# Performance work log

Measured on AMD Instinct MI355X. Metric: run time of the kernel, lower is better.

The kernel has to match this reference:

```python
import jax, jax.numpy as jnp
import numpy as np

B = 131072   # batch of cells
D = 128      # input_dim == number of per-node models
OUTDIM = 2   # predict_var=True -> (delta, var) heads per node


def setup_inputs() -> dict:
    key = jax.random.key(0)
    k1, k2, k3 = jax.random.split(key, 3)
    state = jax.random.normal(k1, (B, D), dtype=jnp.float32)
    # Stacked weights of the D tiny Linear(D, 2) layers: W[n] is node n's [2, D] weight
    W = jax.random.normal(k2, (D, OUTDIM, D), dtype=jnp.float32) * 0.05
    b = jax.random.normal(k3, (D, OUTDIM), dtype=jnp.float32) * 0.05
    return {"state": state, "W": W, "b": b}


def reference(state, W, b):
    # Original: for each node i, y = Linear_i(state) -> delta[:, i] = y[:, 0]; var[:, i] = y[:, 1]
    # Batched equivalent: one einsum over all nodes at once.
    out = jnp.einsum('bd,nod->bno', state, W) + b  # [B, D, 2]
    delta = out[:, :, 0]
    var = out[:, :, 1]
    return delta, var
```

## Files before the change

kernel.cpp:

```cpp
#include <hip/hip_runtime.h>
#include <hip/hip_bf16.h>

typedef __attribute__((ext_vector_type(8))) short bf16x8;
typedef __attribute__((ext_vector_type(4))) float f32x4;

constexpr int BROWS = 131072;
constexpr int DDIM  = 128;

__device__ __forceinline__ short to_bf16(float f) {
    unsigned u = __builtin_bit_cast(unsigned, f);
    u = (u + 0x7FFFu + ((u >> 16) & 1u)) >> 16;
    return (short)u;
}

__device__ __forceinline__ bf16x8 cvt8(const float* __restrict__ p) {
    f32x4 lo = *reinterpret_cast<const f32x4*>(p);
    f32x4 hi = *reinterpret_cast<const f32x4*>(p + 4);
    bf16x8 r;
#pragma unroll
    for (int i = 0; i < 4; ++i) { r[i] = to_bf16(lo[i]); r[i + 4] = to_bf16(hi[i]); }
    return r;
}

__global__ void __launch_bounds__(256)
lfm_kernel(const float* __restrict__ state, const float* __restrict__ W,
           const float* __restrict__ bias, float* __restrict__ out) {
    const int lane = threadIdx.x & 63;
    const int wave = threadIdx.x >> 6;
    const int l16  = lane & 15;
    const int lq   = lane >> 4;

    const int colbase = wave * 64;
    bf16x8 wfrag[4][4];
    float  biasr[4];
#pragma unroll
    for (int ct = 0; ct < 4; ++ct) {
        const int c = colbase + ct * 16 + l16;
        const int n = c & 127, o = c >> 7;
        const float* wrow = W + n * 256 + o * 128;
        biasr[ct] = bias[n * 2 + o];
#pragma unroll
        for (int ks = 0; ks < 4; ++ks)
            wfrag[ct][ks] = cvt8(wrow + ks * 32 + lq * 8);
    }

    const int ntiles = BROWS / 16;
    for (int t = blockIdx.x; t < ntiles; t += gridDim.x) {
        const float* srow = state + (size_t)(t * 16 + l16) * DDIM;
        bf16x8 afrag[4];
#pragma unroll
        for (int ks = 0; ks < 4; ++ks)
            afrag[ks] = cvt8(srow + ks * 32 + lq * 8);

#pragma unroll
        for (int ct = 0; ct < 4; ++ct) {
            f32x4 acc = { biasr[ct], biasr[ct], biasr[ct], biasr[ct] };
#pragma unroll
            for (int ks = 0; ks < 4; ++ks)
                acc = __builtin_amdgcn_mfma_f32_16x16x32_bf16(
                        afrag[ks], wfrag[ct][ks], acc, 0, 0, 0);

            const int c = colbase + ct * 16 + l16;
            const size_t row = (size_t)t * 16 + lq * 4;
            float* dst = out + ((c < 128)
                                ? (row * 128 + c)
                                : ((size_t)BROWS * 128 + row * 128 + (c - 128)));
#pragma unroll
            for (int r = 0; r < 4; ++r)
                dst[(size_t)r * 128] = acc[r];
        }
    }
}

extern "C" void kernel_launch(void* const* d_in, const int* in_sizes, int n_in,
                              void* d_out, int out_size, void* d_ws, size_t ws_size,
                              hipStream_t stream) {
    const float* state = (const float*)d_in[0];
    const float* W     = (const float*)d_in[1];
    const float* bias  = (const float*)d_in[2];
    float* out = (float*)d_out;
    hipLaunchKernelGGL(lfm_kernel, dim3(2048), dim3(256), 0, stream,
                       state, W, bias, out);
}
```

Measured before the change: 221.9 us.

## Split output planes across blocks, swap MFMA operands for vector stores, double-buffer loads

Each block now handles only one output plane (delta or var), so each wave holds half the weight fragments. Swapping the MFMA operand order makes each lane own four contiguous output columns, which allows 16-byte vector stores in place of strided scalar stores. The tile loop is fully unrolled with two raw fp32 register buffers, so the next tile's state loads are in flight during the current tile's compute. The cost is that every state row is now read by two blocks, relying on L2 to absorb the duplicate traffic, and the code hardcodes an exact iteration count per block.

```diff
diff --git a/kernel.cpp b/kernel.cpp
--- a/kernel.cpp
+++ b/kernel.cpp
@@ -1,11 +1,13 @@
 #include <hip/hip_runtime.h>
-#include <hip/hip_bf16.h>
 
 typedef __attribute__((ext_vector_type(8))) short bf16x8;
 typedef __attribute__((ext_vector_type(4))) float f32x4;
 
 constexpr int BROWS = 131072;
 constexpr int DDIM  = 128;
+constexpr int NTILES = BROWS / 16;
+constexpr int CLSBLOCKS = 2048;
+constexpr int ITERS = NTILES / CLSBLOCKS;
 
 __device__ __forceinline__ short to_bf16(float f) {
     unsigned u = __builtin_bit_cast(unsigned, f);
@@ -13,16 +15,14 @@
     return (short)u;
 }
 
-__device__ __forceinline__ bf16x8 cvt8(const float* __restrict__ p) {
-    f32x4 lo = *reinterpret_cast<const f32x4*>(p);
-    f32x4 hi = *reinterpret_cast<const f32x4*>(p + 4);
+__device__ __forceinline__ bf16x8 cvt8(f32x4 lo, f32x4 hi) {
     bf16x8 r;
 #pragma unroll
     for (int i = 0; i < 4; ++i) { r[i] = to_bf16(lo[i]); r[i + 4] = to_bf16(hi[i]); }
     return r;
 }
 
-__global__ void __launch_bounds__(256)
+__global__ void __launch_bounds__(256, 4)
 lfm_kernel(const float* __restrict__ state, const float* __restrict__ W,
            const float* __restrict__ bias, float* __restrict__ out) {
     const int lane = threadIdx.x & 63;
@@ -30,46 +30,61 @@
     const int l16  = lane & 15;
     const int lq   = lane >> 4;
 
-    const int colbase = wave * 64;
-    bf16x8 wfrag[4][4];
-    float  biasr[4];
+    const int cls = blockIdx.x & 1;
+    const int tb  = blockIdx.x >> 1;
+    const int colbase = wave * 32;
+
+    bf16x8 wfrag[2][4];
+    f32x4  bias4[2];
 #pragma unroll
-    for (int ct = 0; ct < 4; ++ct) {
-        const int c = colbase + ct * 16 + l16;
-        const int n = c & 127, o = c >> 7;
-        const float* wrow = W + n * 256 + o * 128;
-        biasr[ct] = bias[n * 2 + o];
+    for (int ct = 0; ct < 2; ++ct) {
+        const int n = colbase + ct * 16 + l16;
+        const float* wrow = W + n * 256 + cls * 128;
 #pragma unroll
-        for (int ks = 0; ks < 4; ++ks)
-            wfrag[ct][ks] = cvt8(wrow + ks * 32 + lq * 8);
+        for (int ks = 0; ks < 4; ++ks) {
+            f32x4 lo = *reinterpret_cast<const f32x4*>(wrow + ks * 32 + lq * 8);
+            f32x4 hi = *reinterpret_cast<const f32x4*>(wrow + ks * 32 + lq * 8 + 4);
+            wfrag[ct][ks] = cvt8(lo, hi);
+        }
+        const int c0 = colbase + ct * 16 + lq * 4;
+#pragma unroll
+        for (int r = 0; r < 4; ++r)
+            bias4[ct][r] = bias[(c0 + r) * 2 + cls];
     }
 
-    const int ntiles = BROWS / 16;
-    for (int t = blockIdx.x; t < ntiles; t += gridDim.x) {
-        const float* srow = state + (size_t)(t * 16 + l16) * DDIM;
-        bf16x8 afrag[4];
-#pragma unroll
-        for (int ks = 0; ks < 4; ++ks)
-            afrag[ks] = cvt8(srow + ks * 32 + lq * 8);
+    float* oplane = out + (size_t)cls * BROWS * 128;
 
-#pragma unroll
-        for (int ct = 0; ct < 4; ++ct) {
-            f32x4 acc = { biasr[ct], biasr[ct], biasr[ct], biasr[ct] };
-#pragma unroll
-            for (int ks = 0; ks < 4; ++ks)
-                acc = __builtin_amdgcn_mfma_f32_16x16x32_bf16(
-                        afrag[ks], wfrag[ct][ks], acc, 0, 0, 0);
+#define LOADT(BUF, T) { \
+    const float* srow = state + ((size_t)((T) * 16 + l16)) * DDIM + lq * 8; \
+    _Pragma("unroll") \
+    for (int ks = 0; ks < 4; ++ks) { \
+        BUF[2 * ks]     = *reinterpret_cast<const f32x4*>(srow + ks * 32); \
+        BUF[2 * ks + 1] = *reinterpret_cast<const f32x4*>(srow + ks * 32 + 4); \
+    } }
 
-            const int c = colbase + ct * 16 + l16;
-            const size_t row = (size_t)t * 16 + lq * 4;
-            float* dst = out + ((c < 128)
-                                ? (row * 128 + c)
-                                : ((size_t)BROWS * 128 + row * 128 + (c - 128)));
-#pragma unroll
-            for (int r = 0; r < 4; ++r)
-                dst[(size_t)r * 128] = acc[r];
-        }
-    }
+#define COMPUTE(BUF, T) { \
+    f32x4 acc0 = bias4[0], acc1 = bias4[1]; \
+    _Pragma("unroll") \
+    for (int ks = 0; ks < 4; ++ks) { \
+        bf16x8 af = cvt8(BUF[2 * ks], BUF[2 * ks + 1]); \
+        acc0 = __builtin_amdgcn_mfma_f32_16x16x32_bf16(wfrag[0][ks], af, acc0, 0, 0, 0); \
+        acc1 = __builtin_amdgcn_mfma_f32_16x16x32_bf16(wfrag[1][ks], af, acc1, 0, 0, 0); \
+    } \
+    float* orow = oplane + ((size_t)((T) * 16 + l16)) * 128; \
+    *reinterpret_cast<f32x4*>(orow + colbase + lq * 4)      = acc0; \
+    *reinterpret_cast<f32x4*>(orow + colbase + 16 + lq * 4) = acc1; }
+
+    f32x4 rawA[8], rawB[8];
+    LOADT(rawA, tb)
+    LOADT(rawB, (tb + CLSBLOCKS))
+    COMPUTE(rawA, tb)
+    LOADT(rawA, (tb + 2 * CLSBLOCKS))
+    COMPUTE(rawB, (tb + CLSBLOCKS))
+    LOADT(rawB, (tb + 3 * CLSBLOCKS))
+    COMPUTE(rawA, (tb + 2 * CLSBLOCKS))
+    COMPUTE(rawB, (tb + 3 * CLSBLOCKS))
+#undef LOADT
+#undef COMPUTE
 }
 
 extern "C" void kernel_launch(void* const* d_in, const int* in_sizes, int n_in,
@@ -79,6 +94,6 @@
     const float* W     = (const float*)d_in[1];
     const float* bias  = (const float*)d_in[2];
     float* out = (float*)d_out;
-    hipLaunchKernelGGL(lfm_kernel, dim3(2048), dim3(256), 0, stream,
+    hipLaunchKernelGGL(lfm_kernel, dim3(2 * CLSBLOCKS), dim3(256), 0, stream,
                        state, W, bias, out);
 }
```

After: 251.9 us. +13.5%, slower.
